# Optimization experiments

Hardware: AMD Instinct MI355X
Metric: run time of the kernel (lower is better)

Reference implementation:

```python
import jax, jax.numpy as jnp
import numpy as np

H = 256
H2 = H // 2
N = 1024
T = 12
B = 4


def setup_inputs() -> dict:
    key = jax.random.key(0)
    ks = jax.random.split(key, 12)
    s = lambda fan_in: 1.0 / np.sqrt(fan_in)
    inp = {
        "node_embeddings": jax.random.normal(ks[0], (B, N, H), jnp.float32),
        # origin encoder: Linear(H,H) -> ReLU -> Linear(H,H2)
        "W1o": jax.random.normal(ks[1], (H, H), jnp.float32) * s(H),
        "b1o": jnp.zeros((H,), jnp.float32),
        "W2o": jax.random.normal(ks[2], (H, H2), jnp.float32) * s(H),
        "b2o": jnp.zeros((H2,), jnp.float32),
        # dest encoder
        "W1d": jax.random.normal(ks[3], (H, H), jnp.float32) * s(H),
        "b1d": jnp.zeros((H,), jnp.float32),
        "W2d": jax.random.normal(ks[4], (H, H2), jnp.float32) * s(H),
        "b2d": jnp.zeros((H2,), jnp.float32),
        # bilinear: out = o @ Wb @ d^T + bb  (torch nn.Bilinear(H2,H2,1))
        "Wb": jax.random.normal(ks[5], (H2, H2), jnp.float32) * s(H2),
        "bb": jnp.zeros((), jnp.float32),
        # horizon predictor: Linear(1, T) -> ReLU
        "wh": jax.random.normal(ks[6], (T,), jnp.float32),
        "bh": jnp.zeros((T,), jnp.float32),
    }
    return inp


def reference(node_embeddings, W1o, b1o, W2o, b2o, W1d, b1d, W2d, b2d, Wb, bb, wh, bh):
    # encoders (dropout is identity at eval)
    o = jax.nn.relu(node_embeddings @ W1o + b1o) @ W2o + b2o      # (B,N,H2)
    d = jax.nn.relu(node_embeddings @ W1d + b1d) @ W2d + b2d      # (B,N,H2)
    # bilinear score without materializing (B,N,N,H2):
    oW = jnp.einsum("bik,kl->bil", o, Wb)                          # (B,N,H2)
    scores = jnp.einsum("bil,bjl->bij", oW, d) + bb                # (B,N,N)
    # horizon predictor Linear(1,T)+ReLU, then permute to (B,T,N,N)
    pred = jax.nn.relu(scores[..., None] * wh + bh)                # (B,N,N,T)
    pred = jnp.transpose(pred, (0, 3, 1, 2))                       # (B,T,N,N)
    return jax.nn.relu(pred)
```

## Files before the change

### kernel.cpp

```cpp
#include <hip/hip_runtime.h>

constexpr int H  = 256;
constexpr int H2 = 128;
constexpr int N  = 1024;
constexpr int T  = 12;
constexpr int B  = 4;
constexpr int M  = B * N;

__global__ void fold_wb_kernel(const float* __restrict__ W2o,
                               const float* __restrict__ b2o,
                               const float* __restrict__ Wb,
                               float* __restrict__ W2of,
                               float* __restrict__ b2of) {
    __shared__ float row[H2];
    const int i = blockIdx.x;
    const int j = threadIdx.x;
    const float* src = (i < H) ? (W2o + i * H2) : b2o;
    row[j] = src[j];
    __syncthreads();
    float acc = 0.f;
#pragma unroll 8
    for (int k = 0; k < H2; ++k) acc = fmaf(row[k], Wb[k * H2 + j], acc);
    if (i < H) W2of[i * H2 + j] = acc;
    else       b2of[j] = acc;
}

template<bool RELU, int BK>
__global__ __launch_bounds__(256) void gemm_bias_kernel(
    const float* __restrict__ A0, const float* __restrict__ A1,
    const float* __restrict__ W0, const float* __restrict__ W1,
    const float* __restrict__ bias0, const float* __restrict__ bias1,
    float* __restrict__ C0, float* __restrict__ C1,
    int Nout, int K)
{
    const int br = blockIdx.z;
    const float* A    = br ? A1 : A0;
    const float* W    = br ? W1 : W0;
    const float* bias = br ? bias1 : bias0;
    float*       C    = br ? C1 : C0;

    __shared__ float As[BK][68];
    __shared__ float Ws[BK][68];

    const int tid = threadIdx.x;
    const int tx = tid & 15;
    const int ty = tid >> 4;
    const int row0 = blockIdx.y * 64;
    const int col0 = blockIdx.x * 64;

    float acc[4][4] = {};

    for (int kt = 0; kt < K; kt += BK) {
#pragma unroll
        for (int p = 0; p < (64 * BK / 4) / 256; ++p) {
            const int idx = tid + p * 256;
            const int r  = idx / (BK / 4);
            const int c4 = idx % (BK / 4);
            const float4 v = *(const float4*)(A + (size_t)(row0 + r) * K + kt + 4 * c4);
            As[4 * c4 + 0][r] = v.x;
            As[4 * c4 + 1][r] = v.y;
            As[4 * c4 + 2][r] = v.z;
            As[4 * c4 + 3][r] = v.w;
        }
#pragma unroll
        for (int p = 0; p < (BK * 64 / 4) / 256; ++p) {
            const int idx = tid + p * 256;
            const int r  = idx / 16;
            const int c4 = idx % 16;
            *(float4*)&Ws[r][4 * c4] =
                *(const float4*)(W + (size_t)(kt + r) * Nout + col0 + 4 * c4);
        }
        __syncthreads();
#pragma unroll
        for (int k = 0; k < BK; ++k) {
            const float4 a4 = *(const float4*)&As[k][4 * ty];
            const float4 b4 = *(const float4*)&Ws[k][4 * tx];
            const float a[4] = {a4.x, a4.y, a4.z, a4.w};
            const float b[4] = {b4.x, b4.y, b4.z, b4.w};
#pragma unroll
            for (int i = 0; i < 4; ++i)
#pragma unroll
                for (int j = 0; j < 4; ++j)
                    acc[i][j] = fmaf(a[i], b[j], acc[i][j]);
        }
        __syncthreads();
    }

    const float4 bias4 = *(const float4*)(bias + col0 + 4 * tx);
    const float bj[4] = {bias4.x, bias4.y, bias4.z, bias4.w};
#pragma unroll
    for (int i = 0; i < 4; ++i) {
        float4 o;
        float v0 = acc[i][0] + bj[0];
        float v1 = acc[i][1] + bj[1];
        float v2 = acc[i][2] + bj[2];
        float v3 = acc[i][3] + bj[3];
        if (RELU) {
            v0 = fmaxf(v0, 0.f); v1 = fmaxf(v1, 0.f);
            v2 = fmaxf(v2, 0.f); v3 = fmaxf(v3, 0.f);
        }
        o.x = v0; o.y = v1; o.z = v2; o.w = v3;
        *(float4*)(C + (size_t)(row0 + 4 * ty + i) * Nout + col0 + 4 * tx) = o;
    }
}

template<int BK>
__global__ __launch_bounds__(256) void scores_expand_kernel(
    const float* __restrict__ oW, const float* __restrict__ dd,
    const float* __restrict__ bbp, const float* __restrict__ wh,
    const float* __restrict__ bh, float* __restrict__ out)
{
    __shared__ float As[BK][68];
    __shared__ float Bs[BK][68];
    const int tid = threadIdx.x;
    const int tx = tid & 15;
    const int ty = tid >> 4;
    const int b  = blockIdx.z;
    const int i0 = blockIdx.y * 64;
    const int j0 = blockIdx.x * 64;
    const float* Ab = oW + (size_t)b * N * H2;
    const float* Bb = dd + (size_t)b * N * H2;

    float acc[4][4] = {};

    for (int kt = 0; kt < H2; kt += BK) {
#pragma unroll
        for (int p = 0; p < (64 * BK / 4) / 256; ++p) {
            const int idx = tid + p * 256;
            const int r  = idx / (BK / 4);
            const int c4 = idx % (BK / 4);
            const float4 v = *(const float4*)(Ab + (size_t)(i0 + r) * H2 + kt + 4 * c4);
            As[4 * c4 + 0][r] = v.x;
            As[4 * c4 + 1][r] = v.y;
            As[4 * c4 + 2][r] = v.z;
            As[4 * c4 + 3][r] = v.w;
            const float4 w = *(const float4*)(Bb + (size_t)(j0 + r) * H2 + kt + 4 * c4);
            Bs[4 * c4 + 0][r] = w.x;
            Bs[4 * c4 + 1][r] = w.y;
            Bs[4 * c4 + 2][r] = w.z;
            Bs[4 * c4 + 3][r] = w.w;
        }
        __syncthreads();
#pragma unroll
        for (int k = 0; k < BK; ++k) {
            const float4 a4 = *(const float4*)&As[k][4 * ty];
            const float4 b4 = *(const float4*)&Bs[k][4 * tx];
            const float a[4] = {a4.x, a4.y, a4.z, a4.w};
            const float bfr[4] = {b4.x, b4.y, b4.z, b4.w};
#pragma unroll
            for (int i = 0; i < 4; ++i)
#pragma unroll
                for (int j = 0; j < 4; ++j)
                    acc[i][j] = fmaf(a[i], bfr[j], acc[i][j]);
        }
        __syncthreads();
    }

    const float bbv = bbp[0];
    float whr[T], bhr[T];
#pragma unroll
    for (int t = 0; t < T; ++t) { whr[t] = wh[t]; bhr[t] = bh[t]; }

#pragma unroll
    for (int i = 0; i < 4; ++i)
#pragma unroll
        for (int j = 0; j < 4; ++j)
            acc[i][j] += bbv;

#pragma unroll
    for (int t = 0; t < T; ++t) {
        float* obase = out + ((size_t)(b * T + t) * N + i0 + 4 * ty) * N + j0 + 4 * tx;
#pragma unroll
        for (int i = 0; i < 4; ++i) {
            float4 o;
            o.x = fmaxf(fmaf(acc[i][0], whr[t], bhr[t]), 0.f);
            o.y = fmaxf(fmaf(acc[i][1], whr[t], bhr[t]), 0.f);
            o.z = fmaxf(fmaf(acc[i][2], whr[t], bhr[t]), 0.f);
            o.w = fmaxf(fmaf(acc[i][3], whr[t], bhr[t]), 0.f);
            *(float4*)(obase + (size_t)i * N) = o;
        }
    }
}

extern "C" void kernel_launch(void* const* d_in, const int* in_sizes, int n_in,
                              void* d_out, int out_size, void* d_ws, size_t ws_size,
                              hipStream_t stream) {
    const float* x   = (const float*)d_in[0];
    const float* W1o = (const float*)d_in[1];
    const float* b1o = (const float*)d_in[2];
    const float* W2o = (const float*)d_in[3];
    const float* b2o = (const float*)d_in[4];
    const float* W1d = (const float*)d_in[5];
    const float* b1d = (const float*)d_in[6];
    const float* W2d = (const float*)d_in[7];
    const float* b2d = (const float*)d_in[8];
    const float* Wb  = (const float*)d_in[9];
    const float* bb  = (const float*)d_in[10];
    const float* wh  = (const float*)d_in[11];
    const float* bh  = (const float*)d_in[12];
    float* out = (float*)d_out;

    float* ws   = (float*)d_ws;
    float* W2of = ws;
    float* b2of = W2of + H * H2;
    float* oW   = b2of + H2;
    float* dd   = oW + (size_t)M * H2;
    float* h_o  = dd + (size_t)M * H2;
    float* h_d  = h_o + (size_t)M * H;

    fold_wb_kernel<<<H + 1, H2, 0, stream>>>(W2o, b2o, Wb, W2of, b2of);

    gemm_bias_kernel<true, 32><<<dim3(H / 64, M / 64, 2), 256, 0, stream>>>(
        x, x, W1o, W1d, b1o, b1d, h_o, h_d, H, H);

    gemm_bias_kernel<false, 32><<<dim3(H2 / 64, M / 64, 2), 256, 0, stream>>>(
        h_o, h_d, W2of, W2d, b2of, b2d, oW, dd, H2, H);

    scores_expand_kernel<64><<<dim3(N / 64, N / 64, B), 256, 0, stream>>>(
        oW, dd, bb, wh, bh, out);
}
```

Before: 274.5 us.

## Register-prefetch next K-tile in GEMMs, raise BK to 64, interleave encoder outputs

Adds register double-buffering to all three tiled GEMMs: the next K-tile is loaded from global memory into registers while the current shared-memory tile is being computed. This removes one barrier per iteration and hides load latency. The encoder GEMMs move from BK=32 to BK=64, and the origin and destination hidden activations now share one interleaved 512-wide buffer with explicit leading dimensions. The runtime is dominated by the output write of the scores kernel, so the gain may be small, and the extra prefetch registers may lower occupancy.

```diff
diff --git a/kernel.cpp b/kernel.cpp
--- a/kernel.cpp
+++ b/kernel.cpp
@@ -25,52 +25,59 @@
     else       b2of[j] = acc;
 }
 
-template<bool RELU, int BK>
-__global__ __launch_bounds__(256) void gemm_bias_kernel(
-    const float* __restrict__ A0, const float* __restrict__ A1,
-    const float* __restrict__ W0, const float* __restrict__ W1,
-    const float* __restrict__ bias0, const float* __restrict__ bias1,
-    float* __restrict__ C0, float* __restrict__ C1,
-    int Nout, int K)
-{
-    const int br = blockIdx.z;
-    const float* A    = br ? A1 : A0;
-    const float* W    = br ? W1 : W0;
-    const float* bias = br ? bias1 : bias0;
-    float*       C    = br ? C1 : C0;
-
+template<bool RELU>
+__device__ __forceinline__ void gemm_body(
+    const float* __restrict__ A, int lda,
+    const float* __restrict__ W, int ldw,
+    const float* __restrict__ bias,
+    float* __restrict__ C, int ldc,
+    int K)
+{
+    constexpr int BK = 64;
     __shared__ float As[BK][68];
     __shared__ float Ws[BK][68];
 
     const int tid = threadIdx.x;
     const int tx = tid & 15;
     const int ty = tid >> 4;
-    const int row0 = blockIdx.y * 64;
-    const int col0 = blockIdx.x * 64;
+
+    float4 aR[4], wR[4];
+#pragma unroll
+    for (int p = 0; p < 4; ++p) {
+        const int idx = tid + p * 256;
+        const int r  = idx >> 4;
+        const int c4 = idx & 15;
+        aR[p] = *(const float4*)(A + (size_t)r * lda + 4 * c4);
+        wR[p] = *(const float4*)(W + (size_t)r * ldw + 4 * c4);
+    }
 
     float acc[4][4] = {};
 
-    for (int kt = 0; kt < K; kt += BK) {
-#pragma unroll
-        for (int p = 0; p < (64 * BK / 4) / 256; ++p) {
+    const int NK = K / BK;
+    for (int t = 0; t < BK * NK; t += BK) {
+        if (t) __syncthreads();
+#pragma unroll
+        for (int p = 0; p < 4; ++p) {
             const int idx = tid + p * 256;
-            const int r  = idx / (BK / 4);
-            const int c4 = idx % (BK / 4);
-            const float4 v = *(const float4*)(A + (size_t)(row0 + r) * K + kt + 4 * c4);
-            As[4 * c4 + 0][r] = v.x;
-            As[4 * c4 + 1][r] = v.y;
-            As[4 * c4 + 2][r] = v.z;
-            As[4 * c4 + 3][r] = v.w;
-        }
-#pragma unroll
-        for (int p = 0; p < (BK * 64 / 4) / 256; ++p) {
-            const int idx = tid + p * 256;
-            const int r  = idx / 16;
-            const int c4 = idx % 16;
-            *(float4*)&Ws[r][4 * c4] =
-                *(const float4*)(W + (size_t)(kt + r) * Nout + col0 + 4 * c4);
+            const int r  = idx >> 4;
+            const int c4 = idx & 15;
+            As[4 * c4 + 0][r] = aR[p].x;
+            As[4 * c4 + 1][r] = aR[p].y;
+            As[4 * c4 + 2][r] = aR[p].z;
+            As[4 * c4 + 3][r] = aR[p].w;
+            *(float4*)&Ws[r][4 * c4] = wR[p];
         }
         __syncthreads();
+        if (t + BK < K) {
+#pragma unroll
+            for (int p = 0; p < 4; ++p) {
+                const int idx = tid + p * 256;
+                const int r  = idx >> 4;
+                const int c4 = idx & 15;
+                aR[p] = *(const float4*)(A + (size_t)r * lda + t + BK + 4 * c4);
+                wR[p] = *(const float4*)(W + (size_t)(t + BK + r) * ldw + 4 * c4);
+            }
+        }
 #pragma unroll
         for (int k = 0; k < BK; ++k) {
             const float4 a4 = *(const float4*)&As[k][4 * ty];
@@ -83,14 +90,12 @@
                 for (int j = 0; j < 4; ++j)
                     acc[i][j] = fmaf(a[i], b[j], acc[i][j]);
         }
-        __syncthreads();
-    }
-
-    const float4 bias4 = *(const float4*)(bias + col0 + 4 * tx);
-    const float bj[4] = {bias4.x, bias4.y, bias4.z, bias4.w};
+    }
+
+    const float4 b4 = *(const float4*)(bias + 4 * tx);
+    const float bj[4] = {b4.x, b4.y, b4.z, b4.w};
 #pragma unroll
     for (int i = 0; i < 4; ++i) {
-        float4 o;
         float v0 = acc[i][0] + bj[0];
         float v1 = acc[i][1] + bj[1];
         float v2 = acc[i][2] + bj[2];
@@ -99,68 +104,118 @@
             v0 = fmaxf(v0, 0.f); v1 = fmaxf(v1, 0.f);
             v2 = fmaxf(v2, 0.f); v3 = fmaxf(v3, 0.f);
         }
-        o.x = v0; o.y = v1; o.z = v2; o.w = v3;
-        *(float4*)(C + (size_t)(row0 + 4 * ty + i) * Nout + col0 + 4 * tx) = o;
-    }
-}
-
-template<int BK>
+        float4 o; o.x = v0; o.y = v1; o.z = v2; o.w = v3;
+        *(float4*)(C + (size_t)(4 * ty + i) * ldc + 4 * tx) = o;
+    }
+}
+
+__global__ __launch_bounds__(256) void enc1_kernel(
+    const float* __restrict__ x,
+    const float* __restrict__ W1o, const float* __restrict__ W1d,
+    const float* __restrict__ b1o, const float* __restrict__ b1d,
+    float* __restrict__ h)
+{
+    const int bx = blockIdx.x;
+    const int row0 = blockIdx.y * 64;
+    const float* W    = (bx < 4) ? W1o : W1d;
+    const float* bias = (bx < 4) ? b1o : b1d;
+    const int wcol0 = (bx & 3) * 64;
+    gemm_body<true>(x + (size_t)row0 * H, H,
+                    W + wcol0, H,
+                    bias + wcol0,
+                    h + (size_t)row0 * 512 + bx * 64, 512,
+                    H);
+}
+
+__global__ __launch_bounds__(256) void enc2_kernel(
+    const float* __restrict__ h,
+    const float* __restrict__ W2of, const float* __restrict__ b2of,
+    const float* __restrict__ W2d,  const float* __restrict__ b2d,
+    float* __restrict__ oW, float* __restrict__ dd)
+{
+    const int bx = blockIdx.x;
+    const int z = bx >> 1;
+    const int row0 = blockIdx.y * 64;
+    const int wcol0 = (bx & 1) * 64;
+    const float* A    = h + (size_t)row0 * 512 + z * 256;
+    const float* W    = (z ? W2d : W2of) + wcol0;
+    const float* bias = (z ? b2d : b2of) + wcol0;
+    float*       C    = (z ? dd : oW) + (size_t)row0 * H2 + wcol0;
+    gemm_body<false>(A, 512, W, H2, bias, C, H2, H);
+}
+
 __global__ __launch_bounds__(256) void scores_expand_kernel(
     const float* __restrict__ oW, const float* __restrict__ dd,
     const float* __restrict__ bbp, const float* __restrict__ wh,
     const float* __restrict__ bh, float* __restrict__ out)
 {
+    constexpr int BK = 64;
     __shared__ float As[BK][68];
     __shared__ float Bs[BK][68];
+
     const int tid = threadIdx.x;
     const int tx = tid & 15;
     const int ty = tid >> 4;
     const int b  = blockIdx.z;
     const int i0 = blockIdx.y * 64;
     const int j0 = blockIdx.x * 64;
-    const float* Ab = oW + (size_t)b * N * H2;
-    const float* Bb = dd + (size_t)b * N * H2;
+    const float* Ab = oW + (size_t)b * N * H2 + (size_t)i0 * H2;
+    const float* Bb = dd + (size_t)b * N * H2 + (size_t)j0 * H2;
+
+    float4 aR[4], bR[4];
+#pragma unroll
+    for (int p = 0; p < 4; ++p) {
+        const int idx = tid + p * 256;
+        const int r  = idx >> 4;
+        const int c4 = idx & 15;
+        aR[p] = *(const float4*)(Ab + (size_t)r * H2 + 4 * c4);
+        bR[p] = *(const float4*)(Bb + (size_t)r * H2 + 4 * c4);
+    }
 
     float acc[4][4] = {};
 
-    for (int kt = 0; kt < H2; kt += BK) {
-#pragma unroll
-        for (int p = 0; p < (64 * BK / 4) / 256; ++p) {
+    for (int t = 0; t < H2; t += BK) {
+        if (t) __syncthreads();
+#pragma unroll
+        for (int p = 0; p < 4; ++p) {
             const int idx = tid + p * 256;
-            const int r  = idx / (BK / 4);
-            const int c4 = idx % (BK / 4);
-            const float4 v = *(const float4*)(Ab + (size_t)(i0 + r) * H2 + kt + 4 * c4);
-            As[4 * c4 + 0][r] = v.x;
-            As[4 * c4 + 1][r] = v.y;
-            As[4 * c4 + 2][r] = v.z;
-            As[4 * c4 + 3][r] = v.w;
-            const float4 w = *(const float4*)(Bb + (size_t)(j0 + r) * H2 + kt + 4 * c4);
-            Bs[4 * c4 + 0][r] = w.x;
-            Bs[4 * c4 + 1][r] = w.y;
-            Bs[4 * c4 + 2][r] = w.z;
-            Bs[4 * c4 + 3][r] = w.w;
+            const int r  = idx >> 4;
+            const int c4 = idx & 15;
+            As[4 * c4 + 0][r] = aR[p].x;
+            As[4 * c4 + 1][r] = aR[p].y;
+            As[4 * c4 + 2][r] = aR[p].z;
+            As[4 * c4 + 3][r] = aR[p].w;
+            Bs[4 * c4 + 0][r] = bR[p].x;
+            Bs[4 * c4 + 1][r] = bR[p].y;
+            Bs[4 * c4 + 2][r] = bR[p].z;
+            Bs[4 * c4 + 3][r] = bR[p].w;
         }
         __syncthreads();
+        if (t + BK < H2) {
+#pragma unroll
+            for (int p = 0; p < 4; ++p) {
+                const int idx = tid + p * 256;
+                const int r  = idx >> 4;
+                const int c4 = idx & 15;
+                aR[p] = *(const float4*)(Ab + (size_t)r * H2 + t + BK + 4 * c4);
+                bR[p] = *(const float4*)(Bb + (size_t)r * H2 + t + BK + 4 * c4);
+            }
+        }
 #pragma unroll
         for (int k = 0; k < BK; ++k) {
             const float4 a4 = *(const float4*)&As[k][4 * ty];
             const float4 b4 = *(const float4*)&Bs[k][4 * tx];
             const float a[4] = {a4.x, a4.y, a4.z, a4.w};
-            const float bfr[4] = {b4.x, b4.y, b4.z, b4.w};
+            const float bf[4] = {b4.x, b4.y, b4.z, b4.w};
 #pragma unroll
             for (int i = 0; i < 4; ++i)
 #pragma unroll
                 for (int j = 0; j < 4; ++j)
-                    acc[i][j] = fmaf(a[i], bfr[j], acc[i][j]);
-        }
-        __syncthreads();
+                    acc[i][j] = fmaf(a[i], bf[j], acc[i][j]);
+        }
     }
 
     const float bbv = bbp[0];
-    float whr[T], bhr[T];
-#pragma unroll
-    for (int t = 0; t < T; ++t) { whr[t] = wh[t]; bhr[t] = bh[t]; }
-
 #pragma unroll
     for (int i = 0; i < 4; ++i)
 #pragma unroll
@@ -169,15 +224,17 @@
 
 #pragma unroll
     for (int t = 0; t < T; ++t) {
-        float* obase = out + ((size_t)(b * T + t) * N + i0 + 4 * ty) * N + j0 + 4 * tx;
+        const float w = wh[t];
+        const float bhv = bh[t];
+        float* ob = out + ((size_t)(b * T + t) * N + i0 + 4 * ty) * N + j0 + 4 * tx;
 #pragma unroll
         for (int i = 0; i < 4; ++i) {
             float4 o;
-            o.x = fmaxf(fmaf(acc[i][0], whr[t], bhr[t]), 0.f);
-            o.y = fmaxf(fmaf(acc[i][1], whr[t], bhr[t]), 0.f);
-            o.z = fmaxf(fmaf(acc[i][2], whr[t], bhr[t]), 0.f);
-            o.w = fmaxf(fmaf(acc[i][3], whr[t], bhr[t]), 0.f);
-            *(float4*)(obase + (size_t)i * N) = o;
+            o.x = fmaxf(fmaf(acc[i][0], w, bhv), 0.f);
+            o.y = fmaxf(fmaf(acc[i][1], w, bhv), 0.f);
+            o.z = fmaxf(fmaf(acc[i][2], w, bhv), 0.f);
+            o.w = fmaxf(fmaf(acc[i][3], w, bhv), 0.f);
+            *(float4*)(ob + (size_t)i * N) = o;
         }
     }
 }
@@ -205,17 +262,14 @@
     float* b2of = W2of + H * H2;
     float* oW   = b2of + H2;
     float* dd   = oW + (size_t)M * H2;
-    float* h_o  = dd + (size_t)M * H2;
-    float* h_d  = h_o + (size_t)M * H;
+    float* h    = dd + (size_t)M * H2;
 
     fold_wb_kernel<<<H + 1, H2, 0, stream>>>(W2o, b2o, Wb, W2of, b2of);
 
-    gemm_bias_kernel<true, 32><<<dim3(H / 64, M / 64, 2), 256, 0, stream>>>(
-        x, x, W1o, W1d, b1o, b1d, h_o, h_d, H, H);
-
-    gemm_bias_kernel<false, 32><<<dim3(H2 / 64, M / 64, 2), 256, 0, stream>>>(
-        h_o, h_d, W2of, W2d, b2of, b2d, oW, dd, H2, H);
-
-    scores_expand_kernel<64><<<dim3(N / 64, N / 64, B), 256, 0, stream>>>(
+    enc1_kernel<<<dim3(8, M / 64), 256, 0, stream>>>(x, W1o, W1d, b1o, b1d, h);
+
+    enc2_kernel<<<dim3(4, M / 64), 256, 0, stream>>>(h, W2of, b2of, W2d, b2d, oW, dd);
+
+    scores_expand_kernel<<<dim3(N / 64, N / 64, B), 256, 0, stream>>>(
         oW, dd, bb, wh, bh, out);
 }
```

After: 282.5 us. 1.03x slower.
